# Kernel optimization log

Hardware: AMD Instinct MI355X
Metric: run time of the kernel (lower is better)

## Reference

```python
import jax, jax.numpy as jnp
import numpy as np

N_NODES = 50000
NNZ = 1_600_000
D_FEAT = 256


def setup_inputs() -> dict:
    key = jax.random.key(0)
    k_x, k_v, k_r, k_c = jax.random.split(key, 4)
    x = jax.random.normal(k_x, (N_NODES, D_FEAT), dtype=jnp.float32)
    # learned per-nonzero values; torch init uses std = 1/sqrt(mean col degree)
    std = 1.0 / np.sqrt(NNZ / N_NODES)
    values = jax.random.normal(k_v, (NNZ,), dtype=jnp.float32) * std
    row = jax.random.randint(k_r, (NNZ,), 0, N_NODES, dtype=jnp.int64)
    col = jax.random.randint(k_c, (NNZ,), 0, N_NODES, dtype=jnp.int64)
    return {"x": x, "values": values, "row": row, "col": col}


def reference(x, values, row, col):
    # Math identical to matmul(to_dense(coo(row, col, values)), x):
    # out[r] = sum over edges e with row[e]==r of values[e] * x[col[e]]
    msgs = values[:, None] * x[col]            # [nnz, F]
    out = jax.ops.segment_sum(msgs, row, num_segments=N_NODES)  # [N, F]
    return out
```

## Files before the change

kernel.cpp:

```cpp
#include <hip/hip_runtime.h>
#include <hip/hip_bf16.h>


#define FEAT 256
#define CAP 128
#define SCAN_CHUNK 2048

static __device__ __forceinline__ unsigned short f2bf(float f) {
    unsigned int u = __float_as_uint(f);
    u += 0x7FFF + ((u >> 16) & 1);
    return (unsigned short)(u >> 16);
}
static __device__ __forceinline__ float bf2f(unsigned short h) {
    return __uint_as_float(((unsigned int)h) << 16);
}


__global__ __launch_bounds__(256) void prep_kernel(const float4* __restrict__ x4,
                                                   ushort4* __restrict__ xh,
                                                   const int* __restrict__ row,
                                                   const int* __restrict__ col,
                                                   const float* __restrict__ vals,
                                                   int* __restrict__ deg,
                                                   unsigned long long* __restrict__ pack,
                                                   int n4, int nnz) {
    const int stride = gridDim.x * blockDim.x;
    const int tid = blockIdx.x * blockDim.x + threadIdx.x;
    for (int i = tid; i < n4; i += stride) {
        float4 v = x4[i];
        ushort4 o;
        o.x = f2bf(v.x); o.y = f2bf(v.y); o.z = f2bf(v.z); o.w = f2bf(v.w);
        xh[i] = o;
    }
    for (int e = tid; e < nnz; e += stride) {
        int r = row[e];
        int c = col[e];
        float v = vals[e];
        int pos = atomicAdd(&deg[r], 1);
        if (pos < CAP) {
            unsigned long long pr = ((unsigned long long)__float_as_uint(v) << 32)
                                  | (unsigned int)c;
            pack[(size_t)r * CAP + pos] = pr;
        }
    }
}

__global__ __launch_bounds__(256) void spmm_split_kernel(const ushort2* __restrict__ xh2,
                                                         const unsigned long long* __restrict__ pack,
                                                         const int* __restrict__ deg,
                                                         float* __restrict__ out, int n) {
    const int wave = threadIdx.x >> 6;
    const int lane = threadIdx.x & 63;
    const int w = blockIdx.x * 4 + wave;
    const int r = w >> 1;
    const int half = w & 1;
    if (r >= n) return;
    int d = deg[r]; if (d > CAP) d = CAP;
    const unsigned long long* __restrict__ bucket = pack + (size_t)r * CAP;
    const int fofs = half * 64 + lane;
    float2 acc = make_float2(0.f, 0.f);
    for (int k0 = 0; k0 < d; k0 += 64) {
        int cnt = d - k0; if (cnt > 64) cnt = 64;
        float myv = 0.f; int myc = 0;
        if (lane < cnt) {
            unsigned long long pr = __builtin_nontemporal_load(&bucket[k0 + lane]);
            myc = (int)(unsigned int)(pr & 0xFFFFFFFFu);
            myv = __uint_as_float((unsigned int)(pr >> 32));
        }
        for (int j = 0; j < cnt; j += 8) {
            ushort2 h[8];
            float vv[8];
            #pragma unroll
            for (int k = 0; k < 8; ++k) {
                int sidx = j + k; if (sidx > 63) sidx = 63;
                int cc = __builtin_amdgcn_readlane(myc, sidx);
                vv[k] = __uint_as_float(__builtin_amdgcn_readlane(__float_as_uint(myv), sidx));
                h[k] = xh2[(size_t)cc * 128 + fofs];
            }
            #pragma unroll
            for (int k = 0; k < 8; ++k) {
                acc.x += vv[k] * bf2f(h[k].x);
                acc.y += vv[k] * bf2f(h[k].y);
            }
        }
    }
    ((float2*)out)[(size_t)r * 128 + fofs] = acc;
}


__global__ void convx_kernel(const float4* __restrict__ x, ushort4* __restrict__ xh, int n4) {
    int stride = gridDim.x * blockDim.x;
    for (int i = blockIdx.x * blockDim.x + threadIdx.x; i < n4; i += stride) {
        float4 v = x[i];
        ushort4 o;
        o.x = f2bf(v.x); o.y = f2bf(v.y); o.z = f2bf(v.z); o.w = f2bf(v.w);
        xh[i] = o;
    }
}

__global__ void hist_rank_kernel(const int* __restrict__ row, int* __restrict__ deg,
                                 int* __restrict__ rank, int nnz) {
    int stride = gridDim.x * blockDim.x;
    for (int e = blockIdx.x * blockDim.x + threadIdx.x; e < nnz; e += stride) {
        rank[e] = atomicAdd(&deg[row[e]], 1);
    }
}

__global__ __launch_bounds__(256) void scan_chunks_kernel(const int* __restrict__ deg,
                                                          int* __restrict__ rowstart,
                                                          int* __restrict__ partials, int n) {
    __shared__ int s[256];
    const int tid = threadIdx.x;
    const int base = blockIdx.x * SCAN_CHUNK + tid * 8;
    int items[8];
    int sum = 0;
    #pragma unroll
    for (int j = 0; j < 8; ++j) {
        int v = (base + j < n) ? deg[base + j] : 0;
        items[j] = sum;
        sum += v;
    }
    s[tid] = sum;
    __syncthreads();
    for (int off = 1; off < 256; off <<= 1) {
        int t = (tid >= off) ? s[tid - off] : 0;
        __syncthreads();
        s[tid] += t;
        __syncthreads();
    }
    int thread_prefix = s[tid] - sum;
    if (tid == 255) partials[blockIdx.x] = s[255];
    #pragma unroll
    for (int j = 0; j < 8; ++j) {
        if (base + j < n) rowstart[base + j] = items[j] + thread_prefix;
    }
}

__global__ __launch_bounds__(256) void finalize_scan_kernel(int* __restrict__ rowstart,
                                                            const int* __restrict__ partials,
                                                            int n, int nnz) {
    __shared__ int sprefix;
    const int cb = (int)((blockIdx.x * 256u) / SCAN_CHUNK);
    if (threadIdx.x < 64) {
        int v = (threadIdx.x < cb) ? partials[threadIdx.x] : 0;
        #pragma unroll
        for (int off = 32; off; off >>= 1) v += __shfl_down(v, off);
        if (threadIdx.x == 0) sprefix = v;
    }
    __syncthreads();
    int i = blockIdx.x * 256 + threadIdx.x;
    if (i < n) rowstart[i] += sprefix;
    if (i == 0) rowstart[n] = nnz;
}

__global__ void scatter_pack_kernel(const int* __restrict__ row, const int* __restrict__ rank,
                                    const int* __restrict__ col, const float* __restrict__ vals,
                                    const int* __restrict__ rowstart, int2* __restrict__ pack,
                                    int nnz) {
    int stride = gridDim.x * blockDim.x;
    for (int e = blockIdx.x * blockDim.x + threadIdx.x; e < nnz; e += stride) {
        int p = rowstart[row[e]] + rank[e];
        pack[p] = make_int2(col[e], __float_as_int(vals[e]));
    }
}

__global__ __launch_bounds__(256) void spmm_bf16_kernel(const ushort4* __restrict__ xh,
                                                        const int2* __restrict__ pack,
                                                        const int* __restrict__ rowstart,
                                                        float* __restrict__ out, int n) {
    const int wave = threadIdx.x >> 6;
    const int lane = threadIdx.x & 63;
    const int r = blockIdx.x * 4 + wave;
    if (r >= n) return;
    const int s = rowstart[r];
    const int e = rowstart[r + 1];
    float4 acc = make_float4(0.f, 0.f, 0.f, 0.f);
    for (int k0 = s; k0 < e; k0 += 64) {
        int cnt = e - k0; if (cnt > 64) cnt = 64;
        float myv = 0.f; int myc = 0;
        if (lane < cnt) {
            int2 pr = pack[k0 + lane];
            myc = pr.x;
            myv = __int_as_float(pr.y);
        }
        for (int j = 0; j < cnt; ++j) {
            float v = __shfl(myv, j);
            int   c = __shfl(myc, j);
            ushort4 h = xh[c * 64 + lane];
            acc.x += v * bf2f(h.x);
            acc.y += v * bf2f(h.y);
            acc.z += v * bf2f(h.z);
            acc.w += v * bf2f(h.w);
        }
    }
    ((float4*)out)[r * 64 + lane] = acc;
}


extern "C" void kernel_launch(void* const* d_in, const int* in_sizes, int n_in,
                              void* d_out, int out_size, void* d_ws, size_t ws_size,
                              hipStream_t stream) {
    const float* x    = (const float*)d_in[0];
    const float* vals = (const float*)d_in[1];
    const int*   row  = (const int*)d_in[2];
    const int*   col  = (const int*)d_in[3];
    float* out = (float*)d_out;

    const int nnz = in_sizes[1];
    const int n   = out_size / FEAT;
    const int nb  = (n + SCAN_CHUNK - 1) / SCAN_CHUNK;

    {
        char* p0 = (char*)d_ws;
        char* p = p0;
        int* deg = (int*)p;            p += (size_t)n * 4;
        p = (char*)((((size_t)p) + 15) & ~(size_t)15);
        unsigned long long* pack = (unsigned long long*)p; p += (size_t)n * CAP * 8;
        ushort4* xh = (ushort4*)p;     p += (size_t)n * FEAT * 2;
        const size_t need = (size_t)(p - p0);
        if (ws_size >= need) {
            const int n4 = n * (FEAT / 4);
            (void)hipMemsetAsync(deg, 0, (size_t)n * 4, stream);
            prep_kernel<<<2048, 256, 0, stream>>>((const float4*)x, xh, row, col, vals,
                                                  deg, pack, n4, nnz);
            const int nwork = n * 2;
            spmm_split_kernel<<<(nwork + 3) / 4, 256, 0, stream>>>((const ushort2*)xh, pack,
                                                                   deg, out, n);
            return;
        }
    }

    {
        char* p0 = (char*)d_ws;
        char* p = p0;
        int* deg      = (int*)p; p += (size_t)n * 4;
        int* rowstart = (int*)p; p += (size_t)(n + 1) * 4;
        int* partials = (int*)p; p += 64 * 4;
        int* rank     = (int*)p; p += (size_t)nnz * 4;
        p = (char*)((((size_t)p) + 7) & ~(size_t)7);
        int2* pack    = (int2*)p; p += (size_t)nnz * 8;
        unsigned short* xh = (unsigned short*)p; p += (size_t)n * FEAT * 2;
        const size_t need = (size_t)(p - p0);
        if (ws_size >= need) {
            (void)hipMemsetAsync(deg, 0, (size_t)n * 4, stream);
            hist_rank_kernel<<<2048, 256, 0, stream>>>(row, deg, rank, nnz);
            convx_kernel<<<2048, 256, 0, stream>>>((const float4*)x, (ushort4*)xh, n * (FEAT / 4));
            scan_chunks_kernel<<<nb, 256, 0, stream>>>(deg, rowstart, partials, n);
            finalize_scan_kernel<<<(n + 255) / 256, 256, 0, stream>>>(rowstart, partials, n, nnz);
            scatter_pack_kernel<<<2048, 256, 0, stream>>>(row, rank, col, vals, rowstart, pack, nnz);
            spmm_bf16_kernel<<<(n + 3) / 4, 256, 0, stream>>>((const ushort4*)xh, pack, rowstart, out, n);
        }
    }
}
```

Baseline: 328.5 us.

## Split prep into bf16 conversion and row-range-grouped edge scatter kernels

Splits the fused prep kernel into a separate x-to-bf16 conversion kernel and a scatter kernel. In the scatter kernel each block handles one edge chunk and one of 8 row-range groups, so the atomics and bucket writes launched together land in a narrower address window. The aim is better L2/TLB locality for the random scatter writes into the large per-row bucket array. In exchange, the row array is read 8 times and there is one extra kernel launch.

```diff
diff --git a/kernel.cpp b/kernel.cpp
--- a/kernel.cpp
+++ b/kernel.cpp
@@ -4,6 +4,8 @@
 
 #define FEAT 256
 #define CAP 128
+#define NGRP 8
+#define NCHUNK 256
 #define SCAN_CHUNK 2048
 
 static __device__ __forceinline__ unsigned short f2bf(float f) {
@@ -16,31 +18,38 @@
 }
 
 
-__global__ __launch_bounds__(256) void prep_kernel(const float4* __restrict__ x4,
-                                                   ushort4* __restrict__ xh,
-                                                   const int* __restrict__ row,
-                                                   const int* __restrict__ col,
-                                                   const float* __restrict__ vals,
-                                                   int* __restrict__ deg,
-                                                   unsigned long long* __restrict__ pack,
-                                                   int n4, int nnz) {
-    const int stride = gridDim.x * blockDim.x;
-    const int tid = blockIdx.x * blockDim.x + threadIdx.x;
-    for (int i = tid; i < n4; i += stride) {
-        float4 v = x4[i];
+__global__ __launch_bounds__(256) void convx_kernel(const float4* __restrict__ x,
+                                                    ushort4* __restrict__ xh, int n4) {
+    int stride = gridDim.x * blockDim.x;
+    for (int i = blockIdx.x * blockDim.x + threadIdx.x; i < n4; i += stride) {
+        float4 v = x[i];
         ushort4 o;
         o.x = f2bf(v.x); o.y = f2bf(v.y); o.z = f2bf(v.z); o.w = f2bf(v.w);
         xh[i] = o;
     }
-    for (int e = tid; e < nnz; e += stride) {
+}
+
+__global__ __launch_bounds__(256) void scatter_grp_kernel(const int* __restrict__ row,
+                                                          const int* __restrict__ col,
+                                                          const float* __restrict__ vals,
+                                                          int* __restrict__ deg,
+                                                          unsigned long long* __restrict__ pack,
+                                                          int n, int nnz, int epc) {
+    const int g = blockIdx.x & (NGRP - 1);
+    const int q = blockIdx.x >> 3;
+    const int r_lo = (int)(((long long)g * n) / NGRP);
+    const int r_hi = (int)(((long long)(g + 1) * n) / NGRP);
+    const int e0 = q * epc;
+    int e1 = e0 + epc; if (e1 > nnz) e1 = nnz;
+    for (int e = e0 + threadIdx.x; e < e1; e += 256) {
         int r = row[e];
-        int c = col[e];
-        float v = vals[e];
-        int pos = atomicAdd(&deg[r], 1);
-        if (pos < CAP) {
-            unsigned long long pr = ((unsigned long long)__float_as_uint(v) << 32)
-                                  | (unsigned int)c;
-            pack[(size_t)r * CAP + pos] = pr;
+        if (r >= r_lo && r < r_hi) {
+            int pos = atomicAdd(&deg[r], 1);
+            if (pos < CAP) {
+                unsigned long long pr = ((unsigned long long)__float_as_uint(vals[e]) << 32)
+                                      | (unsigned int)col[e];
+                pack[(size_t)r * CAP + pos] = pr;
+            }
         }
     }
 }
@@ -88,16 +97,6 @@
 }
 
 
-__global__ void convx_kernel(const float4* __restrict__ x, ushort4* __restrict__ xh, int n4) {
-    int stride = gridDim.x * blockDim.x;
-    for (int i = blockIdx.x * blockDim.x + threadIdx.x; i < n4; i += stride) {
-        float4 v = x[i];
-        ushort4 o;
-        o.x = f2bf(v.x); o.y = f2bf(v.y); o.z = f2bf(v.z); o.w = f2bf(v.w);
-        xh[i] = o;
-    }
-}
-
 __global__ void hist_rank_kernel(const int* __restrict__ row, int* __restrict__ deg,
                                  int* __restrict__ rank, int nnz) {
     int stride = gridDim.x * blockDim.x;
@@ -220,9 +219,11 @@
         const size_t need = (size_t)(p - p0);
         if (ws_size >= need) {
             const int n4 = n * (FEAT / 4);
+            const int epc = (nnz + NCHUNK - 1) / NCHUNK;
             (void)hipMemsetAsync(deg, 0, (size_t)n * 4, stream);
-            prep_kernel<<<2048, 256, 0, stream>>>((const float4*)x, xh, row, col, vals,
-                                                  deg, pack, n4, nnz);
+            convx_kernel<<<2048, 256, 0, stream>>>((const float4*)x, xh, n4);
+            scatter_grp_kernel<<<NGRP * NCHUNK, 256, 0, stream>>>(row, col, vals,
+                                                                  deg, pack, n, nnz, epc);
             const int nwork = n * 2;
             spmm_split_kernel<<<(nwork + 3) / 4, 256, 0, stream>>>((const ushort2*)xh, pack,
                                                                    deg, out, n);
```

New measurement: 309.1 us. 1.06x faster.
